# Kernel tuning notes

Hardware: AMD Instinct MI355X
Metric: run time of the kernel (lower is better)

The kernel has to match this reference:

```python
import jax, jax.numpy as jnp
import numpy as np

GRID_SIZE = 5
SPLINE_ORDER = 3
KSIZE = 3
STRIDE = 1
PAD = 1
NBASES = GRID_SIZE + SPLINE_ORDER  # 8 spline basis functions per input


def _grid():
    # efficient-kan default: grid_range=[-1,1], extended by spline_order knots each side
    h = 2.0 / GRID_SIZE
    return jnp.arange(-SPLINE_ORDER, GRID_SIZE + SPLINE_ORDER + 1, dtype=jnp.float32) * h - 1.0  # [12]


def _b_splines(x, grid):
    # x: [..., ] scalar features -> Cox-de Boor bases [..., NBASES]
    x = x[..., None]
    bases = ((x >= grid[:-1]) & (x < grid[1:])).astype(x.dtype)  # degree-0, [..., 11]
    for k in range(1, SPLINE_ORDER + 1):
        left = (x - grid[: -(k + 1)]) / (grid[k:-1] - grid[: -(k + 1)]) * bases[..., :-1]
        right = (grid[k + 1:] - x) / (grid[k + 1:] - grid[1:-k]) * bases[..., 1:]
        bases = left + right
    return bases  # [..., NBASES]


def _extract_patches(x, k, stride, padding):
    # x: [B,C,H,W] -> [B,C,oh,ow,k*k] patches, matching the torch slicing loop
    if padding > 0:
        x = jnp.pad(x, ((0, 0), (0, 0), (padding, padding), (padding, padding)))
    B, C, H, W = x.shape
    oh = (H - k) // stride + 1
    ow = (W - k) // stride + 1
    cols = [x[:, :, dh:dh + (oh - 1) * stride + 1:stride, dw:dw + (ow - 1) * stride + 1:stride]
            for dh in range(k) for dw in range(k)]
    return jnp.stack(cols, axis=-1)  # row-major (h w) flatten like rearrange 'b h w -> b (h w)'


def setup_inputs() -> dict:
    key = jax.random.key(0)
    ks = jax.random.split(key, 5)
    B, Cin, Cout, H, W = 4, 16, 16, 128, 128
    k2 = KSIZE * KSIZE
    x = jax.random.normal(ks[0], (B, Cin, H, W), dtype=jnp.float32)
    base_weight = jax.random.normal(ks[1], (Cout, Cin, k2, k2), dtype=jnp.float32) * (1.0 / np.sqrt(k2))
    spline_weight = jax.random.normal(ks[2], (Cout, Cin, k2, k2, NBASES), dtype=jnp.float32) * 0.1
    spline_scaler = jax.random.normal(ks[3], (Cout, Cin, k2, k2), dtype=jnp.float32) * (1.0 / np.sqrt(k2))
    bias_weight = jax.random.normal(ks[4], (Cout,), dtype=jnp.float32)
    return {"x": x, "base_weight": base_weight, "spline_weight": spline_weight,
            "spline_scaler": spline_scaler, "bias_weight": bias_weight}


def reference(x, base_weight, spline_weight, spline_scaler, bias_weight):
    # patches: [B, Cin, oh, ow, k2] -- identical for every out-channel i
    patches = _extract_patches(x, KSIZE, STRIDE, PAD)
    grid = _grid()
    bspl = _b_splines(patches, grid)  # [B, Cin, oh, ow, k2, NBASES]
    # KANLinear output is summed over its output dim m, so pre-sum weights over m
    base_w = base_weight.sum(axis=2)                                   # [Cout, Cin, k2]
    spl_w = (spline_weight * spline_scaler[..., None]).sum(axis=2)     # [Cout, Cin, k2, NBASES]
    out = jnp.einsum('bjhwn,ijn->bihw', jax.nn.silu(patches), base_w)
    out = out + jnp.einsum('bjhwns,ijns->bihw', bspl, spl_w)
    out = out + bias_weight[None, :, None, None]
    return out
```

## Files before the change

### kernel.cpp

```cpp
#include <hip/hip_runtime.h>
#include <hip/hip_bf16.h>

#define HW 128

typedef __attribute__((ext_vector_type(8))) short bf16x8;
typedef __attribute__((ext_vector_type(4))) float f32x4;

__device__ __forceinline__ ushort f2bf(float x) {
  uint u = __builtin_bit_cast(uint, x);
  u += 0x7FFFu + ((u >> 16) & 1u);
  return (ushort)(u >> 16);
}
__device__ __forceinline__ uint bpack(float a, float b) {
  return (uint)f2bf(a) | ((uint)f2bf(b) << 16);
}

__global__ __launch_bounds__(64) void kan_prep2(const float* __restrict__ bw,
                                                const float* __restrict__ sw,
                                                const float* __restrict__ sc,
                                                ushort* __restrict__ Wb) {
  __shared__ float sws[648];
  __shared__ float bws[81];
  __shared__ float scs[81];
  int l = threadIdx.x;
  int ij = blockIdx.x;
  int i = ij >> 4, j = ij & 15;
  const float* swp = sw + ij * 648;
  const float* bwp = bw + ij * 81;
  const float* scp = sc + ij * 81;
#pragma unroll
  for (int t = 0; t < 10; ++t) sws[t * 64 + l] = swp[t * 64 + l];
  if (l < 8) sws[640 + l] = swp[640 + l];
  bws[l < 81 ? l : 80] = bwp[l < 81 ? l : 80];
  if (l < 17) bws[64 + l] = bwp[64 + l];
  scs[l < 81 ? l : 80] = scp[l < 81 ? l : 80];
  if (l < 17) scs[64 + l] = scp[64 + l];
  __syncthreads();
#pragma unroll
  for (int r = 0; r < 2; ++r) {
    int o = r * 64 + l;
    if (o < 90) {
      int n = o / 10, c = o % 10;
      float s = 0.f;
      if (c == 0) {
#pragma unroll
        for (int m = 0; m < 9; ++m) s += bws[m * 9 + n];
      } else if (c <= 8) {
#pragma unroll
        for (int m = 0; m < 9; ++m) s += sws[(m * 9 + n) * 8 + (c - 1)] * scs[m * 9 + n];
      }
      int k = j * 10 + c;
      int q = k >> 5, lq = (k >> 3) & 3, e = k & 7;
      int t = n * 5 + q;
      Wb[((t * 16 + i) * 4 + lq) * 8 + e] = f2bf(s);
    }
  }
}

#define PSTRIDE 336
#define HALO_PX 180

__device__ __forceinline__ float bspline_slot(float t, int s) {
  float a = fabsf(t - (float)(s + 2));
  float w = fmaxf(2.0f - a, 0.0f);
  float cube = w * w * w * (1.0f / 6.0f);
  float poly = fmaf(a * a, fmaf(0.5f, a, -1.0f), 2.0f / 3.0f);
  return (a < 1.0f) ? poly : cube;
}

__global__ __launch_bounds__(256, 2) void kan_mfma(
    const float* __restrict__ X, const ushort* __restrict__ Wb,
    const float* __restrict__ bias, float* __restrict__ out) {
  __shared__ char smem[HALO_PX * PSTRIDE];

  int tid = threadIdx.x;
  int lane = tid & 63;
  int wid = tid >> 6;
  int bid = blockIdx.x;
  int b = bid >> 7;
  int tile = bid & 127;
  int h0 = (tile >> 3) << 3;
  int w0 = (tile & 7) << 4;
  int li = lane & 15;
  int lq = lane >> 4;

  const char* wbase = (const char*)Wb + li * 64 + lq * 16;

  bf16x8 Bbuf[15];
#pragma unroll
  for (int t = 0; t < 15; ++t)
    Bbuf[t] = *(const bf16x8*)(wbase + t * 1024);

#pragma unroll
  for (int r = 0; r < 3; ++r) {
    int tq = r * 256 + tid;
    if (tq < 720) {
      int p = tq >> 2, jq = tq & 3;
      int hh = p / 18, ww = p - hh * 18;
      int gh = h0 + hh - 1, gw = w0 + ww - 1;
      bool inb = (gh >= 0) & (gh < HW) & (gw >= 0) & (gw < HW);
      const float* xp = X + ((b * 16 + jq * 4) << 14) + (gh << 7) + gw;
      uint W[20];
#pragma unroll
      for (int jl = 0; jl < 4; ++jl) {
        float xv = inb ? xp[jl << 14] : 0.f;
        float sil = __fdividef(xv, 1.0f + __expf(-xv));
        float t = (xv + 2.2f) * 2.5f;
        float n0 = bspline_slot(t, 0), n1 = bspline_slot(t, 1);
        float n2 = bspline_slot(t, 2), n3 = bspline_slot(t, 3);
        float n4 = bspline_slot(t, 4), n5 = bspline_slot(t, 5);
        float n6 = bspline_slot(t, 6), n7 = bspline_slot(t, 7);
        W[jl * 5 + 0] = bpack(sil, n0);
        W[jl * 5 + 1] = bpack(n1, n2);
        W[jl * 5 + 2] = bpack(n3, n4);
        W[jl * 5 + 3] = bpack(n5, n6);
        W[jl * 5 + 4] = (uint)f2bf(n7);
      }
      char* qp = smem + p * PSTRIDE + jq * 80;
#pragma unroll
      for (int w = 0; w < 5; ++w) {
        uint4 v = make_uint4(W[w * 4 + 0], W[w * 4 + 1], W[w * 4 + 2], W[w * 4 + 3]);
        *reinterpret_cast<uint4*>(qp + w * 16) = v;
      }
    }
  }
  __syncthreads();

  f32x4 acc0 = {0.f, 0.f, 0.f, 0.f};
  f32x4 acc1 = {0.f, 0.f, 0.f, 0.f};
  int ab = li * PSTRIDE + lq * 16;
  const char* base0 = smem + wid * (18 * PSTRIDE) + ab;
  const char* base1 = smem + (wid + 4) * (18 * PSTRIDE) + ab;

#pragma unroll
  for (int s = 0; s < 3; ++s) {
#pragma unroll
    for (int tt = 0; tt < 15; ++tt) {
      const int t = s * 15 + tt;
      const int n = t / 5, q = t - n * 5;
      const int dh = n / 3, dw = n - dh * 3;
      const int imm = (dh * 18 + dw) * PSTRIDE + q * 64;
      bf16x8 a0 = *(const bf16x8*)(base0 + imm);
      acc0 = __builtin_amdgcn_mfma_f32_16x16x32_bf16(a0, Bbuf[tt], acc0, 0, 0, 0);
      bf16x8 a1 = *(const bf16x8*)(base1 + imm);
      acc1 = __builtin_amdgcn_mfma_f32_16x16x32_bf16(a1, Bbuf[tt], acc1, 0, 0, 0);
      if (s < 2)
        Bbuf[tt] = *(const bf16x8*)(wbase + ((s + 1) * 15 + tt) * 1024);
    }
  }

  float bias_v = bias[li];
  float* op0 = out + ((b * 16 + li) << 14) + ((h0 + wid) << 7) + w0 + lq * 4;
  float* op1 = out + ((b * 16 + li) << 14) + ((h0 + wid + 4) << 7) + w0 + lq * 4;
  float4 v0, v1;
  v0.x = acc0[0] + bias_v; v0.y = acc0[1] + bias_v;
  v0.z = acc0[2] + bias_v; v0.w = acc0[3] + bias_v;
  v1.x = acc1[0] + bias_v; v1.y = acc1[1] + bias_v;
  v1.z = acc1[2] + bias_v; v1.w = acc1[3] + bias_v;
  *reinterpret_cast<float4*>(op0) = v0;
  *reinterpret_cast<float4*>(op1) = v1;
}

extern "C" void kernel_launch(void* const* d_in, const int* in_sizes, int n_in,
                              void* d_out, int out_size, void* d_ws, size_t ws_size,
                              hipStream_t stream) {
  const float* x    = (const float*)d_in[0];
  const float* bw   = (const float*)d_in[1];
  const float* sw   = (const float*)d_in[2];
  const float* sc   = (const float*)d_in[3];
  const float* bias = (const float*)d_in[4];
  float* out = (float*)d_out;
  ushort* Wb = (ushort*)d_ws;

  hipLaunchKernelGGL(kan_prep2, dim3(256), dim3(64), 0, stream, bw, sw, sc, Wb);
  hipLaunchKernelGGL(kan_mfma, dim3(512), dim3(256), 0, stream, x, Wb, bias, out);
}
```

Measured before the change: 22.53 us.

## Swizzle LDS patch layout to avoid bank conflicts and preload all weights

Applies an XOR swizzle of 16-byte chunks, keyed on pixel index bit 3, when writing bf16 basis features to shared memory, and applies the matching swizzle on the MFMA operand reads. The aim is to remove LDS bank conflicts caused by the 336-byte pixel stride. All 45 B-fragments are now loaded into registers up front instead of being streamed in three 15-fragment stages, which removes loads from the MFMA loop. Holding 45 fragments raises VGPR pressure, which under launch_bounds(256,2) may cause spills or lower occupancy.

```diff
diff --git a/kernel.cpp b/kernel.cpp
--- a/kernel.cpp
+++ b/kernel.cpp
@@ -2,6 +2,8 @@
 #include <hip/hip_bf16.h>
 
 #define HW 128
+#define PSTRIDE 336
+#define HALO_PX 180
 
 typedef __attribute__((ext_vector_type(8))) short bf16x8;
 typedef __attribute__((ext_vector_type(4))) float f32x4;
@@ -24,17 +26,15 @@
   __shared__ float scs[81];
   int l = threadIdx.x;
   int ij = blockIdx.x;
-  int i = ij >> 4, j = ij & 15;
   const float* swp = sw + ij * 648;
   const float* bwp = bw + ij * 81;
   const float* scp = sc + ij * 81;
 #pragma unroll
   for (int t = 0; t < 10; ++t) sws[t * 64 + l] = swp[t * 64 + l];
   if (l < 8) sws[640 + l] = swp[640 + l];
-  bws[l < 81 ? l : 80] = bwp[l < 81 ? l : 80];
-  if (l < 17) bws[64 + l] = bwp[64 + l];
-  scs[l < 81 ? l : 80] = scp[l < 81 ? l : 80];
-  if (l < 17) scs[64 + l] = scp[64 + l];
+  bws[l] = bwp[l];
+  scs[l] = scp[l];
+  if (l < 17) { bws[64 + l] = bwp[64 + l]; scs[64 + l] = scp[64 + l]; }
   __syncthreads();
 #pragma unroll
   for (int r = 0; r < 2; ++r) {
@@ -49,6 +49,7 @@
 #pragma unroll
         for (int m = 0; m < 9; ++m) s += sws[(m * 9 + n) * 8 + (c - 1)] * scs[m * 9 + n];
       }
+      int i = ij >> 4, j = ij & 15;
       int k = j * 10 + c;
       int q = k >> 5, lq = (k >> 3) & 3, e = k & 7;
       int t = n * 5 + q;
@@ -56,9 +57,6 @@
     }
   }
 }
-
-#define PSTRIDE 336
-#define HALO_PX 180
 
 __device__ __forceinline__ float bspline_slot(float t, int s) {
   float a = fabsf(t - (float)(s + 2));
@@ -71,7 +69,7 @@
 __global__ __launch_bounds__(256, 2) void kan_mfma(
     const float* __restrict__ X, const ushort* __restrict__ Wb,
     const float* __restrict__ bias, float* __restrict__ out) {
-  __shared__ char smem[HALO_PX * PSTRIDE];
+  __shared__ __align__(16) char smem[HALO_PX * PSTRIDE];
 
   int tid = threadIdx.x;
   int lane = tid & 63;
@@ -85,11 +83,10 @@
   int lq = lane >> 4;
 
   const char* wbase = (const char*)Wb + li * 64 + lq * 16;
-
-  bf16x8 Bbuf[15];
+  bf16x8 B[45];
 #pragma unroll
-  for (int t = 0; t < 15; ++t)
-    Bbuf[t] = *(const bf16x8*)(wbase + t * 1024);
+  for (int t = 0; t < 45; ++t)
+    B[t] = *(const bf16x8*)(wbase + t * 1024);
 
 #pragma unroll
   for (int r = 0; r < 3; ++r) {
@@ -116,11 +113,14 @@
         W[jl * 5 + 3] = bpack(n5, n6);
         W[jl * 5 + 4] = (uint)f2bf(n7);
       }
-      char* qp = smem + p * PSTRIDE + jq * 80;
+      char* pix = smem + p * PSTRIDE;
+      uint fp = ((uint)p >> 3) & 1u;
 #pragma unroll
       for (int w = 0; w < 5; ++w) {
+        uint off = (uint)(jq * 80 + w * 16);
+        uint swz = (((off >> 6) ^ fp) & 1u) << 4;
         uint4 v = make_uint4(W[w * 4 + 0], W[w * 4 + 1], W[w * 4 + 2], W[w * 4 + 3]);
-        *reinterpret_cast<uint4*>(qp + w * 16) = v;
+        *reinterpret_cast<uint4*>(pix + (off ^ swz)) = v;
       }
     }
   }
@@ -128,24 +128,27 @@
 
   f32x4 acc0 = {0.f, 0.f, 0.f, 0.f};
   f32x4 acc1 = {0.f, 0.f, 0.f, 0.f};
-  int ab = li * PSTRIDE + lq * 16;
-  const char* base0 = smem + wid * (18 * PSTRIDE) + ab;
-  const char* base1 = smem + (wid + 4) * (18 * PSTRIDE) + ab;
+  uint lqo = (uint)lq * 16u;
 
 #pragma unroll
-  for (int s = 0; s < 3; ++s) {
+  for (int n = 0; n < 9; ++n) {
+    const int dh = n / 3, dw = n % 3;
+    int pr0 = (wid + dh) * 18 + li + dw;
+    int pr1 = pr0 + 72;
+    uint f0 = (((uint)pr0 >> 3) & 1u) << 4;
+    uint f1 = (((uint)pr1 >> 3) & 1u) << 4;
+    uint oE0 = lqo ^ f0, oO0 = oE0 ^ 16u;
+    uint oE1 = lqo ^ f1, oO1 = oE1 ^ 16u;
+    uint b0 = (uint)pr0 * 336u;
+    uint b1 = (uint)pr1 * 336u;
 #pragma unroll
-    for (int tt = 0; tt < 15; ++tt) {
-      const int t = s * 15 + tt;
-      const int n = t / 5, q = t - n * 5;
-      const int dh = n / 3, dw = n - dh * 3;
-      const int imm = (dh * 18 + dw) * PSTRIDE + q * 64;
-      bf16x8 a0 = *(const bf16x8*)(base0 + imm);
-      acc0 = __builtin_amdgcn_mfma_f32_16x16x32_bf16(a0, Bbuf[tt], acc0, 0, 0, 0);
-      bf16x8 a1 = *(const bf16x8*)(base1 + imm);
-      acc1 = __builtin_amdgcn_mfma_f32_16x16x32_bf16(a1, Bbuf[tt], acc1, 0, 0, 0);
-      if (s < 2)
-        Bbuf[tt] = *(const bf16x8*)(wbase + ((s + 1) * 15 + tt) * 1024);
+    for (int q = 0; q < 5; ++q) {
+      uint o0 = b0 + ((q & 1) ? oO0 : oE0) + (uint)(q * 64);
+      uint o1 = b1 + ((q & 1) ? oO1 : oE1) + (uint)(q * 64);
+      bf16x8 a0 = *(const bf16x8*)(smem + o0);
+      acc0 = __builtin_amdgcn_mfma_f32_16x16x32_bf16(a0, B[n * 5 + q], acc0, 0, 0, 0);
+      bf16x8 a1 = *(const bf16x8*)(smem + o1);
+      acc1 = __builtin_amdgcn_mfma_f32_16x16x32_bf16(a1, B[n * 5 + q], acc1, 0, 0, 0);
     }
   }
 
```

Result: slower. 24.55 us (+9.0%).
